# Performance work log

Hardware: AMD Instinct MI355X
Metric: run time of the kernel (lower is better)

## Reference

```python
import jax, jax.numpy as jnp
import numpy as np

IMPOSSIBLE = -10000.0  # DataConfig.IMPOSSIBLE_SCORE
B, L, V, E, H, T = 64, 512, 50000, 256, 512, 32


def setup_inputs() -> dict:
    key = jax.random.key(0)
    ks = jax.random.split(key, 15)
    s = 0.05
    return {
        "sents": jax.random.randint(ks[0], (B, L), 0, V),
        "lengths": jnp.full((B,), L, dtype=jnp.int32),
        "targets": jax.random.randint(ks[1], (B, L, T), 0, 2).astype(jnp.int32),
        "emb": jax.random.normal(ks[2], (V, E), jnp.float32) * s,
        "Wih_f": jax.random.normal(ks[3], (4 * H, E), jnp.float32) * s,
        "Whh_f": jax.random.normal(ks[4], (4 * H, H), jnp.float32) * s,
        "b_f": jax.random.normal(ks[5], (4 * H,), jnp.float32) * s,
        "Wih_b": jax.random.normal(ks[6], (4 * H, E), jnp.float32) * s,
        "Whh_b": jax.random.normal(ks[7], (4 * H, H), jnp.float32) * s,
        "b_b": jax.random.normal(ks[8], (4 * H,), jnp.float32) * s,
        "W_out": jax.random.normal(ks[9], (T, 2 * H), jnp.float32) * s,
        "b_out": jax.random.normal(ks[10], (T,), jnp.float32) * s,
        "start_trans": jax.random.normal(ks[11], (T,), jnp.float32),
        "end_trans": jax.random.normal(ks[12], (T,), jnp.float32),
        "trans": jnp.ones((T, T), jnp.float32) / T,
    }


def _lstm_dir(xW, Whh, reverse):
    # xW: (L, B, 4H) = x @ Wih.T + b, precomputed (the big GEMM, done once)
    h0 = jnp.zeros((xW.shape[1], Whh.shape[1]), xW.dtype)
    def step(carry, xw):
        h, c = carry
        g = xw + h @ Whh.T
        i, f, gg, o = jnp.split(g, 4, axis=-1)  # torch gate order i,f,g,o
        c = jax.nn.sigmoid(f) * c + jax.nn.sigmoid(i) * jnp.tanh(gg)
        h = jax.nn.sigmoid(o) * jnp.tanh(c)
        return (h, c), h
    _, hs = jax.lax.scan(step, (h0, h0), xW, reverse=reverse)
    return hs  # (L, B, H), in original time order


def _denominator(em, trans, start, end):
    # em: (L, B, T); CRF partition function via forward algorithm (mask = all ones)
    alpha0 = start + em[0]
    def step(alpha, e):
        inner = alpha[:, :, None] + trans[None] + e[:, None, :]  # (B, T, T)
        return jax.nn.logsumexp(inner, axis=1), None
    alpha, _ = jax.lax.scan(step, alpha0, em[1:])
    return jax.nn.logsumexp(alpha + end[None, :], axis=-1)  # (B,)


def _numerator(em, pt, trans, start, end):
    # em: (L, B, T); pt: (L, B, T) binary possible-tag mask (float)
    alpha0 = start + em[0]
    alpha0 = jnp.where(pt[0] == 0, IMPOSSIBLE, alpha0)
    def step(alpha, inputs):
        e, cur, nxt = inputs  # each (B, T)
        e = jnp.where(nxt == 0, IMPOSSIBLE, e)
        tr = jnp.where(cur[:, :, None] == 0, IMPOSSIBLE, trans[None])
        tr = jnp.where(nxt[:, None, :] == 0, IMPOSSIBLE, tr)
        inner = alpha[:, :, None] + e[:, None, :] + tr
        return jax.nn.logsumexp(inner, axis=1), None
    alpha, _ = jax.lax.scan(step, alpha0, (em[1:], pt[:-1], pt[1:]))
    et = end[None, :] * pt[-1]
    et = jnp.where(et == 0, IMPOSSIBLE, et)
    return jax.nn.logsumexp(alpha + et, axis=-1)  # (B,)


def reference(sents, lengths, targets, emb, Wih_f, Whh_f, b_f, Wih_b, Whh_b, b_b,
              W_out, b_out, start_trans, end_trans, trans):
    x = emb[sents]                      # (B, L, E)
    x = jnp.transpose(x, (1, 0, 2))     # (L, B, E) time-major
    hf = _lstm_dir(jnp.einsum('lbe,ge->lbg', x, Wih_f) + b_f, Whh_f, False)
    hb = _lstm_dir(jnp.einsum('lbe,ge->lbg', x, Wih_b) + b_b, Whh_b, True)
    em = jnp.einsum('lbh,th->lbt', jnp.concatenate([hf, hb], axis=-1), W_out) + b_out  # (L,B,T)
    pt = jnp.transpose(targets, (1, 0, 2)).astype(em.dtype)  # (L, B, T)
    gold = _numerator(em, pt, trans, start_trans, end_trans)
    fwd = _denominator(em, trans, start_trans, end_trans)
    return jnp.sum(fwd - gold)
```

## Files before the change

kernel.cpp:

```cpp
#include <hip/hip_runtime.h>


#define IMPOSSIBLE -10000.0f
#define CANARY 0x7FFF7FFFu

typedef __attribute__((ext_vector_type(8))) short bf16x8;
typedef __attribute__((ext_vector_type(4))) float f32x4;
typedef __attribute__((ext_vector_type(4))) unsigned int u32x4;
typedef unsigned int u32;
typedef unsigned short u16;

__device__ __forceinline__ u16 f2b(float f) {
  union { float f; u32 u; } v; v.f = f;
  return (u16)((v.u + 0x7fffu + ((v.u >> 16) & 1u)) >> 16);
}
__device__ __forceinline__ float sigm(float x) { return 1.0f / (1.0f + __expf(-x)); }
__device__ __forceinline__ float tanh_f(float x) { return 1.0f - 2.0f / (__expf(2.0f * x) + 1.0f); }

__global__ __launch_bounds__(256) void k_init(u32* __restrict__ H2w,
                                              float* __restrict__ out) {
  const size_t i = ((size_t)blockIdx.x * 256 + threadIdx.x) * 4;
  const uint4 c4 = {CANARY, CANARY, CANARY, CANARY};
  *(uint4*)(H2w + i) = c4;
  if (blockIdx.x == 0 && threadIdx.x == 0)
    __hip_atomic_store((u32*)out, 0u, __ATOMIC_RELAXED, __HIP_MEMORY_SCOPE_AGENT);
}

__global__ __launch_bounds__(256) void k_embed(
    const int* __restrict__ sents, const float* __restrict__ emb,
    u16* __restrict__ x2) {
  __shared__ int tok[64];
  const int tid = threadIdx.x, t = blockIdx.x;
  if (tid < 64) tok[tid] = sents[tid * 512 + t];
  __syncthreads();
#pragma unroll
  for (int i = 0; i < 16; ++i) {
    const int v = i * 256 + tid;
    const int row = v >> 6, ke = (v & 63) * 4;
    const float4 f = *(const float4*)(emb + (size_t)tok[row] * 256 + ke);
    ushort4 s; s.x = f2b(f.x); s.y = f2b(f.y); s.z = f2b(f.z); s.w = f2b(f.w);
    *(ushort4*)&x2[((size_t)t * 64 + row) * 256 + ke] = s;
  }
}

__global__ __launch_bounds__(256, 1) void k_lstm(
    const float* __restrict__ Whf, const float* __restrict__ Whb,
    const float* __restrict__ Wif, const float* __restrict__ Wib,
    const float* __restrict__ bf_, const float* __restrict__ bb_,
    const u16* __restrict__ x2, u16* __restrict__ H2) {
  __shared__ float pre4[4096];
  const int tid = threadIdx.x, wid = blockIdx.x;
  const int r = wid & 7, d = r >> 2, g = r & 3, s = wid >> 3;
  const int b0 = g * 16, j0 = s * 16;
  const float* __restrict__ Whh = d ? Whb : Whf;
  const float* __restrict__ Wih = d ? Wib : Wif;
  const float* __restrict__ bias = d ? bb_ : bf_;
  const int wv = tid >> 6, lane = tid & 63, lm = lane & 15, kh = lane >> 4;
  const int bl = tid >> 4, jj = tid & 15;

  bf16x8 wih_f[8], whh_f[16];
#pragma unroll
  for (int gg = 0; gg < 4; ++gg) {
    const float* wp = Wih + (size_t)(gg * 512 + j0 + lm) * 256 + wv * 64;
#pragma unroll
    for (int kt = 0; kt < 2; ++kt) {
      bf16x8 f;
#pragma unroll
      for (int j = 0; j < 8; ++j) f[j] = (short)f2b(wp[kt * 32 + kh * 8 + j]);
      wih_f[gg * 2 + kt] = f;
    }
    const float* wq = Whh + (size_t)(gg * 512 + j0 + lm) * 512 + wv * 128;
#pragma unroll
    for (int kt = 0; kt < 4; ++kt) {
      bf16x8 f;
#pragma unroll
      for (int j = 0; j < 8; ++j) f[j] = (short)f2b(wq[kt * 32 + kh * 8 + j]);
      whh_f[gg * 4 + kt] = f;
    }
  }
  const float b_i = bias[0 * 512 + j0 + jj];
  const float b_f = bias[1 * 512 + j0 + jj];
  const float b_g = bias[2 * 512 + j0 + jj];
  const float b_o = bias[3 * 512 + j0 + jj];

  float c = 0.f;
  const f32x4 z = {0.f, 0.f, 0.f, 0.f};
#pragma unroll 1
  for (int it = 0; it < 512; ++it) {
    const int tt = d ? (511 - it) : it;
    bf16x8 xa[2];
    {
      const u16* xp = x2 + ((size_t)tt * 64 + b0 + lm) * 256 + wv * 64 + kh * 8;
      xa[0] = *(const bf16x8*)xp;
      xa[1] = *(const bf16x8*)(xp + 32);
    }
    u32x4 q0, q1, q2, q3;
    const u32 *p0, *p1, *p2, *p3;
    if (it > 0) {
      const int tp = d ? (tt + 1) : (tt - 1);
      const size_t tb = (((size_t)tp * 2 + d) * 4 + g) * 32;
      const int fo = lm * 16 + (kh & 1) * 8;
      p0 = (const u32*)(H2 + (tb + wv * 8 + 0 + (kh >> 1)) * 256 + fo);
      p1 = (const u32*)(H2 + (tb + wv * 8 + 2 + (kh >> 1)) * 256 + fo);
      p2 = (const u32*)(H2 + (tb + wv * 8 + 4 + (kh >> 1)) * 256 + fo);
      p3 = (const u32*)(H2 + (tb + wv * 8 + 6 + (kh >> 1)) * 256 + fo);
      asm volatile(
          "global_load_dwordx4 %0, %4, off sc0 sc1\n\t"
          "global_load_dwordx4 %1, %5, off sc0 sc1\n\t"
          "global_load_dwordx4 %2, %6, off sc0 sc1\n\t"
          "global_load_dwordx4 %3, %7, off sc0 sc1"
          : "=&v"(q0), "=&v"(q1), "=&v"(q2), "=&v"(q3)
          : "v"(p0), "v"(p1), "v"(p2), "v"(p3)
          : "memory");
    }
    f32x4 accg[4] = {z, z, z, z};
#pragma unroll
    for (int gg = 0; gg < 4; ++gg)
#pragma unroll
      for (int kt = 0; kt < 2; ++kt)
        accg[gg] = __builtin_amdgcn_mfma_f32_16x16x32_bf16(xa[kt], wih_f[gg * 2 + kt], accg[gg], 0, 0, 0);
    if (it > 0) {
      asm volatile("s_waitcnt vmcnt(0)"
                   : "+v"(q0), "+v"(q1), "+v"(q2), "+v"(q3) :: "memory");
      u32 anybad;
      {
        u32 a0 = (u32)(q0[0] == CANARY) | (u32)(q0[1] == CANARY) |
                 (u32)(q0[2] == CANARY) | (u32)(q0[3] == CANARY);
        u32 a1 = (u32)(q1[0] == CANARY) | (u32)(q1[1] == CANARY) |
                 (u32)(q1[2] == CANARY) | (u32)(q1[3] == CANARY);
        u32 a2 = (u32)(q2[0] == CANARY) | (u32)(q2[1] == CANARY) |
                 (u32)(q2[2] == CANARY) | (u32)(q2[3] == CANARY);
        u32 a3 = (u32)(q3[0] == CANARY) | (u32)(q3[1] == CANARY) |
                 (u32)(q3[2] == CANARY) | (u32)(q3[3] == CANARY);
        anybad = a0 | a1 | a2 | a3;
      }
      int bud = 4096;
      while (__any(anybad != 0) && --bud) {
        asm volatile(
            "global_load_dwordx4 %0, %4, off sc0 sc1\n\t"
            "global_load_dwordx4 %1, %5, off sc0 sc1\n\t"
            "global_load_dwordx4 %2, %6, off sc0 sc1\n\t"
            "global_load_dwordx4 %3, %7, off sc0 sc1\n\t"
            "s_waitcnt vmcnt(0)"
            : "=&v"(q0), "=&v"(q1), "=&v"(q2), "=&v"(q3)
            : "v"(p0), "v"(p1), "v"(p2), "v"(p3)
            : "memory");
        u32 a0 = (u32)(q0[0] == CANARY) | (u32)(q0[1] == CANARY) |
                 (u32)(q0[2] == CANARY) | (u32)(q0[3] == CANARY);
        u32 a1 = (u32)(q1[0] == CANARY) | (u32)(q1[1] == CANARY) |
                 (u32)(q1[2] == CANARY) | (u32)(q1[3] == CANARY);
        u32 a2 = (u32)(q2[0] == CANARY) | (u32)(q2[1] == CANARY) |
                 (u32)(q2[2] == CANARY) | (u32)(q2[3] == CANARY);
        u32 a3 = (u32)(q3[0] == CANARY) | (u32)(q3[1] == CANARY) |
                 (u32)(q3[2] == CANARY) | (u32)(q3[3] == CANARY);
        anybad = a0 | a1 | a2 | a3;
      }
      union { u32x4 q; bf16x8 v; } c0, c1, c2, c3;
      c0.q = q0; c1.q = q1; c2.q = q2; c3.q = q3;
#pragma unroll
      for (int gg = 0; gg < 4; ++gg) {
        accg[gg] = __builtin_amdgcn_mfma_f32_16x16x32_bf16(c0.v, whh_f[gg * 4 + 0], accg[gg], 0, 0, 0);
        accg[gg] = __builtin_amdgcn_mfma_f32_16x16x32_bf16(c1.v, whh_f[gg * 4 + 1], accg[gg], 0, 0, 0);
        accg[gg] = __builtin_amdgcn_mfma_f32_16x16x32_bf16(c2.v, whh_f[gg * 4 + 2], accg[gg], 0, 0, 0);
        accg[gg] = __builtin_amdgcn_mfma_f32_16x16x32_bf16(c3.v, whh_f[gg * 4 + 3], accg[gg], 0, 0, 0);
      }
    }
    __syncthreads();
#pragma unroll
    for (int gg = 0; gg < 4; ++gg)
      *(f32x4*)&pre4[wv * 1024 + gg * 256 + kh * 64 + lm * 4] = accg[gg];
    __syncthreads();
    const int off = (bl >> 2) * 64 + jj * 4 + (bl & 3);
    float pi = b_i, pf = b_f, pg = b_g, po = b_o;
#pragma unroll
    for (int w4 = 0; w4 < 4; ++w4) {
      pi += pre4[w4 * 1024 + 0   + off];
      pf += pre4[w4 * 1024 + 256 + off];
      pg += pre4[w4 * 1024 + 512 + off];
      po += pre4[w4 * 1024 + 768 + off];
    }
    c = sigm(pf) * c + sigm(pi) * tanh_f(pg);
    const float h = sigm(po) * tanh_f(c);
    const float hq = __shfl_xor(h, 1);
    if ((tid & 1) == 0) {
      const u32 pk = (u32)f2b(h) | ((u32)f2b(hq) << 16);
      u32* hp2 = (u32*)H2 + ((((size_t)tt * 2 + d) * 4 + g) * 32 + s) * 128 + (tid >> 1);
      __hip_atomic_store(hp2, pk, __ATOMIC_RELAXED, __HIP_MEMORY_SCOPE_AGENT);
    }
  }
}

__global__ __launch_bounds__(256) void k_emproj(
    const u16* __restrict__ H2, const float* __restrict__ Wo,
    const float* __restrict__ bo, float* __restrict__ em) {
  __shared__ u16 Wl[32 * 1024];
  const int tid = threadIdx.x, mb = blockIdx.x;
  const int wv = tid >> 6, lane = tid & 63, lm = lane & 15, kh = lane >> 4;
#pragma unroll
  for (int i = 0; i < 32; ++i) {
    const int row = i, k = tid * 4;
    const float4 f = *(const float4*)(Wo + (size_t)row * 1024 + k);
    ushort4 s; s.x = f2b(f.x); s.y = f2b(f.y); s.z = f2b(f.z); s.w = f2b(f.w);
    *(ushort4*)&Wl[row * 1024 + ((k + 8 * row) & 1023)] = s;
  }
  __syncthreads();
  const f32x4 z = {0.f, 0.f, 0.f, 0.f};
  f32x4 acc[2] = {z, z};
#pragma unroll 2
  for (int kt = 0; kt < 32; ++kt) {
    const int dd = kt >> 4;
    const int sG = (kt & 15) * 2 + (kh >> 1);
    const u16* ap = H2 + ((((size_t)mb * 2 + dd) * 4 + wv) * 32 + sG) * 256 + lm * 16 + (kh & 1) * 8;
    const bf16x8 a = *(const bf16x8*)ap;
#pragma unroll
    for (int ni = 0; ni < 2; ++ni) {
      const int row = ni * 16 + lm;
      const bf16x8 b = *(const bf16x8*)&Wl[row * 1024 + ((kt * 32 + kh * 8 + 8 * row) & 1023)];
      acc[ni] = __builtin_amdgcn_mfma_f32_16x16x32_bf16(a, b, acc[ni], 0, 0, 0);
    }
  }
#pragma unroll
  for (int ni = 0; ni < 2; ++ni) {
    const int n = ni * 16 + lm;
    const float bv = bo[n];
#pragma unroll
    for (int rr = 0; rr < 4; ++rr) {
      const int m = mb * 64 + wv * 16 + kh * 4 + rr;
      em[(size_t)m * 32 + n] = acc[ni][rr] + bv;
    }
  }
}

__global__ __launch_bounds__(64) void k_crf(
    const float* __restrict__ em, const int* __restrict__ tgt,
    const float* __restrict__ trans, const float* __restrict__ stt,
    const float* __restrict__ ent, float* __restrict__ out) {
  const int lane = threadIdx.x;
  const int b = blockIdx.x >> 1;
  const int isnum = blockIdx.x & 1;
  const int k = lane & 31, j0 = (lane >> 5) * 16;
  float tr[16];
#pragma unroll
  for (int j = 0; j < 16; ++j) tr[j] = trans[(j0 + j) * 32 + k];

  float an; int nxt;
  {
    float a0 = stt[k] + em[(size_t)b * 32 + k];
    int p0 = 1;
    if (isnum) { p0 = tgt[((size_t)b * 512) * 32 + k]; if (p0 == 0) a0 = IMPOSSIBLE; }
    an = a0; nxt = p0;
  }
  u32 cmask = (u32)__ballot(nxt != 0);

  const size_t eb = (size_t)b * 32 + k;
  const size_t tb = (size_t)b * 16384 + k;
  float e1 = em[eb + 1 * 2048], e2 = em[eb + 2 * 2048];
  float e3 = em[eb + 3 * 2048], e4 = em[eb + 4 * 2048];
  int g1 = 1, g2 = 1, g3 = 1, g4 = 1;
  if (isnum) {
    g1 = tgt[tb + 1 * 32]; g2 = tgt[tb + 2 * 32];
    g3 = tgt[tb + 3 * 32]; g4 = tgt[tb + 4 * 32];
  }

  auto step = [&](float e_raw, int nx) {
    const u32 cm = cmask >> j0;
    float vv[16];
#pragma unroll
    for (int j = 0; j < 16; ++j) {
      const float a = __shfl(an, j0 + j);
      float t_ = tr[j];
      if (isnum && ((((cm >> j) & 1u) == 0u) || nx == 0)) t_ = IMPOSSIBLE;
      vv[j] = a + t_;
    }
    const float m0 = fmaxf(fmaxf(fmaxf(vv[0], vv[1]), fmaxf(vv[2], vv[3])),
                           fmaxf(fmaxf(vv[4], vv[5]), fmaxf(vv[6], vv[7])));
    const float m1 = fmaxf(fmaxf(fmaxf(vv[8], vv[9]), fmaxf(vv[10], vv[11])),
                           fmaxf(fmaxf(vv[12], vv[13]), fmaxf(vv[14], vv[15])));
    const float m = fmaxf(m0, m1);
    float ss = 0.f;
#pragma unroll
    for (int j = 0; j < 16; ++j) ss += __expf(vv[j] - m);
    const float m2 = __shfl_xor(m, 32);
    const float s2 = __shfl_xor(ss, 32);
    const float M = fmaxf(m, m2);
    const float S = ss * __expf(m - M) + s2 * __expf(m2 - M);
    const float e = (isnum && nx == 0) ? IMPOSSIBLE : e_raw;
    an = M + __logf(S) + e;
    nxt = nx;
    if (isnum) cmask = (u32)__ballot(nx != 0);
  };

#pragma unroll 1
  for (int t = 1; t <= 505; t += 4) {
    const int t7 = (t + 7 < 512) ? (t + 7) : 511;
    const float n1 = em[eb + (size_t)(t + 4) * 2048];
    const float n2 = em[eb + (size_t)(t + 5) * 2048];
    const float n3 = em[eb + (size_t)(t + 6) * 2048];
    const float n4 = em[eb + (size_t)t7 * 2048];
    int h1 = 1, h2 = 1, h3 = 1, h4 = 1;
    if (isnum) {
      h1 = tgt[tb + (size_t)(t + 4) * 32]; h2 = tgt[tb + (size_t)(t + 5) * 32];
      h3 = tgt[tb + (size_t)(t + 6) * 32]; h4 = tgt[tb + (size_t)t7 * 32];
    }
    step(e1, g1); step(e2, g2); step(e3, g3); step(e4, g4);
    e1 = n1; e2 = n2; e3 = n3; e4 = n4;
    g1 = h1; g2 = h2; g3 = h3; g4 = h4;
  }
  step(e1, g1); step(e2, g2); step(e3, g3);

  float x;
  if (!isnum) {
    x = an + ent[k];
  } else {
    const float et = ent[k] * (float)nxt;
    x = an + ((et == 0.f) ? IMPOSSIBLE : et);
  }
  float m = x;
#pragma unroll
  for (int o = 1; o < 32; o <<= 1) m = fmaxf(m, __shfl_xor(m, o));
  float ss = __expf(x - m);
#pragma unroll
  for (int o = 1; o < 32; o <<= 1) ss += __shfl_xor(ss, o);
  if (lane == 0) {
    const float rr = m + __logf(ss);
    atomicAdd(out, isnum ? -rr : rr);
  }
}

extern "C" void kernel_launch(void* const* d_in, const int* in_sizes, int n_in,
                              void* d_out, int out_size, void* d_ws, size_t ws_size,
                              hipStream_t stream) {
  (void)in_sizes; (void)n_in; (void)out_size; (void)ws_size;
  const int* sents = (const int*)d_in[0];
  const int* tgt = (const int*)d_in[2];
  const float* emb = (const float*)d_in[3];
  const float* Wif = (const float*)d_in[4];
  const float* Whf = (const float*)d_in[5];
  const float* bf_ = (const float*)d_in[6];
  const float* Wib = (const float*)d_in[7];
  const float* Whb = (const float*)d_in[8];
  const float* bb_ = (const float*)d_in[9];
  const float* Wo = (const float*)d_in[10];
  const float* bo = (const float*)d_in[11];
  const float* stt = (const float*)d_in[12];
  const float* ent = (const float*)d_in[13];
  const float* trans = (const float*)d_in[14];
  float* out = (float*)d_out;

  char* ws = (char*)d_ws;
  u16* x2 = (u16*)ws;
  u16* H2 = (u16*)(ws + 16777216ull);
  float* em = (float*)(ws + 83886080ull);

  k_init<<<dim3(16384), dim3(256), 0, stream>>>((u32*)H2, out);
  k_embed<<<dim3(512), dim3(256), 0, stream>>>(sents, emb, x2);
  k_lstm<<<dim3(256), dim3(256), 0, stream>>>(Whf, Whb, Wif, Wib, bf_, bb_, x2, H2);
  k_emproj<<<dim3(512), dim3(256), 0, stream>>>(H2, Wo, bo, em);
  k_crf<<<dim3(128), dim3(64), 0, stream>>>(em, tgt, trans, stt, ent, out);
}
```

Before: 1.487 ms.

## Double-buffer LSTM gate scratch and prefetch next-step inputs and hidden state

Gives the gate pre-activation scratch two LDS buffers so each recurrent step needs one barrier instead of two. The next step's x tile is loaded right after the barrier, and the next step's H loads are issued at the end of the current step. Both are meant to overlap global latency with the cell math and with the write to the previous buffer. The early H loads may return canary values more often, which sends more work to the spin-retry loop. They also add register pressure.

```diff
diff --git a/kernel.cpp b/kernel.cpp
--- a/kernel.cpp
+++ b/kernel.cpp
@@ -16,6 +16,11 @@
 }
 __device__ __forceinline__ float sigm(float x) { return 1.0f / (1.0f + __expf(-x)); }
 __device__ __forceinline__ float tanh_f(float x) { return 1.0f - 2.0f / (__expf(2.0f * x) + 1.0f); }
+
+__device__ __forceinline__ u32 can4(const u32x4& q) {
+  return (u32)(q[0] == CANARY) | (u32)(q[1] == CANARY) |
+         (u32)(q[2] == CANARY) | (u32)(q[3] == CANARY);
+}
 
 __global__ __launch_bounds__(256) void k_init(u32* __restrict__ H2w,
                                               float* __restrict__ out) {
@@ -48,7 +53,7 @@
     const float* __restrict__ Wif, const float* __restrict__ Wib,
     const float* __restrict__ bf_, const float* __restrict__ bb_,
     const u16* __restrict__ x2, u16* __restrict__ H2) {
-  __shared__ float pre4[4096];
+  __shared__ float pre4[2][4096];
   const int tid = threadIdx.x, wid = blockIdx.x;
   const int r = wid & 7, d = r >> 2, g = r & 3, s = wid >> 3;
   const int b0 = g * 16, j0 = s * 16;
@@ -85,55 +90,31 @@
 
   float c = 0.f;
   const f32x4 z = {0.f, 0.f, 0.f, 0.f};
+  int buf = 0;
+
+  bf16x8 xc0, xc1;
+  {
+    const int tt0 = d ? 511 : 0;
+    const u16* xp = x2 + ((size_t)tt0 * 64 + b0 + lm) * 256 + wv * 64 + kh * 8;
+    xc0 = *(const bf16x8*)xp;
+    xc1 = *(const bf16x8*)(xp + 32);
+  }
+  u32x4 q0 = {0, 0, 0, 0}, q1 = {0, 0, 0, 0}, q2 = {0, 0, 0, 0}, q3 = {0, 0, 0, 0};
+  const u32 *p0 = nullptr, *p1 = nullptr, *p2 = nullptr, *p3 = nullptr;
+
 #pragma unroll 1
   for (int it = 0; it < 512; ++it) {
     const int tt = d ? (511 - it) : it;
-    bf16x8 xa[2];
-    {
-      const u16* xp = x2 + ((size_t)tt * 64 + b0 + lm) * 256 + wv * 64 + kh * 8;
-      xa[0] = *(const bf16x8*)xp;
-      xa[1] = *(const bf16x8*)(xp + 32);
-    }
-    u32x4 q0, q1, q2, q3;
-    const u32 *p0, *p1, *p2, *p3;
-    if (it > 0) {
-      const int tp = d ? (tt + 1) : (tt - 1);
-      const size_t tb = (((size_t)tp * 2 + d) * 4 + g) * 32;
-      const int fo = lm * 16 + (kh & 1) * 8;
-      p0 = (const u32*)(H2 + (tb + wv * 8 + 0 + (kh >> 1)) * 256 + fo);
-      p1 = (const u32*)(H2 + (tb + wv * 8 + 2 + (kh >> 1)) * 256 + fo);
-      p2 = (const u32*)(H2 + (tb + wv * 8 + 4 + (kh >> 1)) * 256 + fo);
-      p3 = (const u32*)(H2 + (tb + wv * 8 + 6 + (kh >> 1)) * 256 + fo);
-      asm volatile(
-          "global_load_dwordx4 %0, %4, off sc0 sc1\n\t"
-          "global_load_dwordx4 %1, %5, off sc0 sc1\n\t"
-          "global_load_dwordx4 %2, %6, off sc0 sc1\n\t"
-          "global_load_dwordx4 %3, %7, off sc0 sc1"
-          : "=&v"(q0), "=&v"(q1), "=&v"(q2), "=&v"(q3)
-          : "v"(p0), "v"(p1), "v"(p2), "v"(p3)
-          : "memory");
-    }
     f32x4 accg[4] = {z, z, z, z};
 #pragma unroll
-    for (int gg = 0; gg < 4; ++gg)
-#pragma unroll
-      for (int kt = 0; kt < 2; ++kt)
-        accg[gg] = __builtin_amdgcn_mfma_f32_16x16x32_bf16(xa[kt], wih_f[gg * 2 + kt], accg[gg], 0, 0, 0);
+    for (int gg = 0; gg < 4; ++gg) {
+      accg[gg] = __builtin_amdgcn_mfma_f32_16x16x32_bf16(xc0, wih_f[gg * 2 + 0], accg[gg], 0, 0, 0);
+      accg[gg] = __builtin_amdgcn_mfma_f32_16x16x32_bf16(xc1, wih_f[gg * 2 + 1], accg[gg], 0, 0, 0);
+    }
     if (it > 0) {
       asm volatile("s_waitcnt vmcnt(0)"
                    : "+v"(q0), "+v"(q1), "+v"(q2), "+v"(q3) :: "memory");
-      u32 anybad;
-      {
-        u32 a0 = (u32)(q0[0] == CANARY) | (u32)(q0[1] == CANARY) |
-                 (u32)(q0[2] == CANARY) | (u32)(q0[3] == CANARY);
-        u32 a1 = (u32)(q1[0] == CANARY) | (u32)(q1[1] == CANARY) |
-                 (u32)(q1[2] == CANARY) | (u32)(q1[3] == CANARY);
-        u32 a2 = (u32)(q2[0] == CANARY) | (u32)(q2[1] == CANARY) |
-                 (u32)(q2[2] == CANARY) | (u32)(q2[3] == CANARY);
-        u32 a3 = (u32)(q3[0] == CANARY) | (u32)(q3[1] == CANARY) |
-                 (u32)(q3[2] == CANARY) | (u32)(q3[3] == CANARY);
-        anybad = a0 | a1 | a2 | a3;
-      }
+      u32 anybad = can4(q0) | can4(q1) | can4(q2) | can4(q3);
       int bud = 4096;
       while (__any(anybad != 0) && --bud) {
         asm volatile(
@@ -145,15 +126,7 @@
             : "=&v"(q0), "=&v"(q1), "=&v"(q2), "=&v"(q3)
             : "v"(p0), "v"(p1), "v"(p2), "v"(p3)
             : "memory");
-        u32 a0 = (u32)(q0[0] == CANARY) | (u32)(q0[1] == CANARY) |
-                 (u32)(q0[2] == CANARY) | (u32)(q0[3] == CANARY);
-        u32 a1 = (u32)(q1[0] == CANARY) | (u32)(q1[1] == CANARY) |
-                 (u32)(q1[2] == CANARY) | (u32)(q1[3] == CANARY);
-        u32 a2 = (u32)(q2[0] == CANARY) | (u32)(q2[1] == CANARY) |
-                 (u32)(q2[2] == CANARY) | (u32)(q2[3] == CANARY);
-        u32 a3 = (u32)(q3[0] == CANARY) | (u32)(q3[1] == CANARY) |
-                 (u32)(q3[2] == CANARY) | (u32)(q3[3] == CANARY);
-        anybad = a0 | a1 | a2 | a3;
+        anybad = can4(q0) | can4(q1) | can4(q2) | can4(q3);
       }
       union { u32x4 q; bf16x8 v; } c0, c1, c2, c3;
       c0.q = q0; c1.q = q1; c2.q = q2; c3.q = q3;
@@ -165,19 +138,24 @@
         accg[gg] = __builtin_amdgcn_mfma_f32_16x16x32_bf16(c3.v, whh_f[gg * 4 + 3], accg[gg], 0, 0, 0);
       }
     }
+#pragma unroll
+    for (int gg = 0; gg < 4; ++gg)
+      *(f32x4*)&pre4[buf][wv * 1024 + gg * 256 + kh * 64 + lm * 4] = accg[gg];
     __syncthreads();
-#pragma unroll
-    for (int gg = 0; gg < 4; ++gg)
-      *(f32x4*)&pre4[wv * 1024 + gg * 256 + kh * 64 + lm * 4] = accg[gg];
-    __syncthreads();
+    if (it < 511) {
+      const int ttn = d ? (tt - 1) : (tt + 1);
+      const u16* xp = x2 + ((size_t)ttn * 64 + b0 + lm) * 256 + wv * 64 + kh * 8;
+      xc0 = *(const bf16x8*)xp;
+      xc1 = *(const bf16x8*)(xp + 32);
+    }
     const int off = (bl >> 2) * 64 + jj * 4 + (bl & 3);
     float pi = b_i, pf = b_f, pg = b_g, po = b_o;
 #pragma unroll
     for (int w4 = 0; w4 < 4; ++w4) {
-      pi += pre4[w4 * 1024 + 0   + off];
-      pf += pre4[w4 * 1024 + 256 + off];
-      pg += pre4[w4 * 1024 + 512 + off];
-      po += pre4[w4 * 1024 + 768 + off];
+      pi += pre4[buf][w4 * 1024 + 0   + off];
+      pf += pre4[buf][w4 * 1024 + 256 + off];
+      pg += pre4[buf][w4 * 1024 + 512 + off];
+      po += pre4[buf][w4 * 1024 + 768 + off];
     }
     c = sigm(pf) * c + sigm(pi) * tanh_f(pg);
     const float h = sigm(po) * tanh_f(c);
@@ -187,6 +165,23 @@
       u32* hp2 = (u32*)H2 + ((((size_t)tt * 2 + d) * 4 + g) * 32 + s) * 128 + (tid >> 1);
       __hip_atomic_store(hp2, pk, __ATOMIC_RELAXED, __HIP_MEMORY_SCOPE_AGENT);
     }
+    if (it < 511) {
+      const size_t tb2 = (((size_t)tt * 2 + d) * 4 + g) * 32;
+      const int fo = lm * 16 + (kh & 1) * 8;
+      p0 = (const u32*)(H2 + (tb2 + wv * 8 + 0 + (kh >> 1)) * 256 + fo);
+      p1 = (const u32*)(H2 + (tb2 + wv * 8 + 2 + (kh >> 1)) * 256 + fo);
+      p2 = (const u32*)(H2 + (tb2 + wv * 8 + 4 + (kh >> 1)) * 256 + fo);
+      p3 = (const u32*)(H2 + (tb2 + wv * 8 + 6 + (kh >> 1)) * 256 + fo);
+      asm volatile(
+          "global_load_dwordx4 %0, %4, off sc0 sc1\n\t"
+          "global_load_dwordx4 %1, %5, off sc0 sc1\n\t"
+          "global_load_dwordx4 %2, %6, off sc0 sc1\n\t"
+          "global_load_dwordx4 %3, %7, off sc0 sc1"
+          : "=&v"(q0), "=&v"(q1), "=&v"(q2), "=&v"(q3)
+          : "v"(p0), "v"(p1), "v"(p2), "v"(p3)
+          : "memory");
+    }
+    buf ^= 1;
   }
 }
 
```

Result: slower. 1.941 ms (+30.6%).
